# Kernel optimization log

Hardware: AMD Instinct MI355X
Metric: run time of the kernel (lower is better)

The kernel has to match this reference:

```python
import jax, jax.numpy as jnp
import numpy as np

IN_DIM = 4
H_DIM = 128
OBS_LEN = 15
PRED_LEN = 15
BATCH = 32768


def _lstm_cell(x, h, c, Wih, Whh, bih, bhh):
    # PyTorch gate order: i, f, g, o
    gates = x @ Wih.T + h @ Whh.T + (bih + bhh)  # [B, 4H]
    i, f, g, o = jnp.split(gates, 4, axis=-1)
    c_new = jax.nn.sigmoid(f) * c + jax.nn.sigmoid(i) * jnp.tanh(g)
    h_new = jax.nn.sigmoid(o) * jnp.tanh(c_new)
    return h_new, c_new


def setup_inputs() -> dict:
    key = jax.random.key(0)
    ks = jax.random.split(key, 12)
    s = 1.0 / np.sqrt(H_DIM)  # PyTorch LSTM/Linear uniform init bound
    u = lambda k, shape: jax.random.uniform(k, shape, jnp.float32, -s, s)
    return {
        "x": jax.random.normal(ks[0], (BATCH, OBS_LEN, IN_DIM), jnp.float32),
        "enc_Wih": u(ks[1], (4 * H_DIM, IN_DIM)),
        "enc_Whh": u(ks[2], (4 * H_DIM, H_DIM)),
        "enc_bih": u(ks[3], (4 * H_DIM,)),
        "enc_bhh": u(ks[4], (4 * H_DIM,)),
        "dec_Wih": u(ks[5], (4 * H_DIM, IN_DIM)),
        "dec_Whh": u(ks[6], (4 * H_DIM, H_DIM)),
        "dec_bih": u(ks[7], (4 * H_DIM,)),
        "dec_bhh": u(ks[8], (4 * H_DIM,)),
        "out_W": u(ks[9], (IN_DIM, H_DIM)),
        "out_b": u(ks[10], (IN_DIM,)),
    }


def reference(x, enc_Wih, enc_Whh, enc_bih, enc_bhh,
              dec_Wih, dec_Whh, dec_bih, dec_bhh, out_W, out_b):
    B = x.shape[0]
    h0 = jnp.zeros((B, H_DIM), x.dtype)
    c0 = jnp.zeros((B, H_DIM), x.dtype)

    # ---- encode: run LSTM over time, keep final h ----
    def enc_step(carry, xt):
        h, c = carry
        h, c = _lstm_cell(xt, h, c, enc_Wih, enc_Whh, enc_bih, enc_bhh)
        return (h, c), None

    (h_enc, _), _ = jax.lax.scan(enc_step, (h0, c0), jnp.swapaxes(x, 0, 1))

    def dec_step(carry, _):
        x0, h, c = carry
        h, c = _lstm_cell(x0, h, c, dec_Wih, dec_Whh, dec_bih, dec_bhh)
        x0 = h @ out_W.T + out_b  # [B, IN_DIM]
        return (x0, h, c), x0

    x0 = x[:, -1, :]
    _, preds = jax.lax.scan(dec_step, (x0, h_enc, h_enc), None, length=PRED_LEN)
    return jnp.swapaxes(preds, 0, 1)  # [B, PRED_LEN, IN_DIM]
```

## Files before the change

kernel.cpp:

```cpp
#include <hip/hip_runtime.h>

#define HD   128
#define SEQ  15
#define BN   32
#define LDH  168
#define KT   5
#define NTHR 512

typedef __bf16 bf16x8 __attribute__((ext_vector_type(8)));
typedef unsigned short us8 __attribute__((ext_vector_type(8)));
typedef float f32x4 __attribute__((ext_vector_type(4)));

__device__ __forceinline__ unsigned short f2bf(float f) {
  unsigned int u = __builtin_bit_cast(unsigned int, f);
  u += 0x7fffu + ((u >> 16) & 1u);
  return (unsigned short)(u >> 16);
}
__device__ __forceinline__ float bfl(unsigned int u) { return __builtin_bit_cast(float, u << 16); }
__device__ __forceinline__ float bfh(unsigned int u) { return __builtin_bit_cast(float, u & 0xffff0000u); }
__device__ __forceinline__ float sigm(float v) { return __builtin_amdgcn_rcpf(1.0f + __expf(-v)); }
__device__ __forceinline__ float tanh_(float v) { return 1.0f - 2.0f * __builtin_amdgcn_rcpf(1.0f + __expf(2.0f * v)); }

__global__ __launch_bounds__(NTHR, 2) void lstm_encdec_kernel(
    const float* __restrict__ x,
    const float* __restrict__ eWih, const float* __restrict__ eWhh,
    const float* __restrict__ ebih, const float* __restrict__ ebhh,
    const float* __restrict__ dWih, const float* __restrict__ dWhh,
    const float* __restrict__ dbih, const float* __restrict__ dbhh,
    const float* __restrict__ oW,  const float* __restrict__ ob,
    float* __restrict__ out)
{
  const int tid  = (int)threadIdx.x;
  const int wv   = tid >> 6;
  const int lane = tid & 63;
  const int l15  = lane & 15;
  const int lk   = lane >> 4;
  const int b0   = (int)blockIdx.x * BN;

  const int pv = tid >> 2, pb = pv >> 2, pd = pv & 3, pq = tid & 3;

  __shared__ alignas(16) unsigned short hb[2][BN][LDH];
  __shared__ alignas(16) unsigned short xbuf[BN][68];
  __shared__ alignas(16) float obuf[BN][68];
  __shared__ float ow_l[4][133];
  __shared__ float ob_l[4];

  bf16x8 bw[4][KT];
  f32x4  cst[2], hst[2];

  for (int i = tid; i < 2 * BN * LDH; i += NTHR) ((unsigned short*)hb)[i] = 0;
  #pragma unroll
  for (int m = 0; m < 2; ++m)
    #pragma unroll
    for (int j = 0; j < 4; ++j) { cst[m][j] = 0.0f; hst[m][j] = 0.0f; }

  auto load_w = [&](const float* Wih, const float* Whh,
                    const float* bih, const float* bhh, bool fold) {
    #pragma unroll
    for (int g = 0; g < 4; ++g) {
      const int gc = g * HD + wv * 16 + l15;
      float wi[4];
      #pragma unroll
      for (int d = 0; d < 4; ++d) wi[d] = Wih[gc * 4 + d];
      float bb = bih[gc] + bhh[gc];
      if (fold) {
        #pragma unroll
        for (int d = 0; d < 4; ++d) bb += ob[d] * wi[d];
      }
      #pragma unroll
      for (int kt = 0; kt < KT - 1; ++kt) {
        const int k0 = kt * 32 + lk * 8;
        const float4* p = (const float4*)&Whh[(size_t)gc * HD + k0];
        const float4 u0 = p[0], u1 = p[1];
        float v[8] = {u0.x, u0.y, u0.z, u0.w, u1.x, u1.y, u1.z, u1.w};
        if (fold) {
          #pragma unroll
          for (int j = 0; j < 8; ++j) {
            float s = v[j];
            #pragma unroll
            for (int d = 0; d < 4; ++d) s += wi[d] * oW[d * HD + k0 + j];
            v[j] = s;
          }
        }
        us8 u;
        #pragma unroll
        for (int j = 0; j < 8; ++j) u[j] = f2bf(v[j]);
        bw[g][kt] = __builtin_bit_cast(bf16x8, u);
      }
      us8 u4 = {0, 0, 0, 0, 0, 0, 0, 0};
      if (lk == 0) {
        #pragma unroll
        for (int j = 0; j < 4; ++j) u4[j] = f2bf(wi[j]);
        const unsigned short bh = f2bf(bb);
        u4[4] = bh;
        u4[5] = f2bf(bb - bfl((unsigned)bh));
      }
      bw[g][KT - 1] = __builtin_bit_cast(bf16x8, u4);
    }
  };

  auto mfma_step = [&](f32x4 (&acc)[2][4], int p) {
    #pragma unroll
    for (int m = 0; m < 2; ++m)
      #pragma unroll
      for (int g = 0; g < 4; ++g)
        #pragma unroll
        for (int j = 0; j < 4; ++j) acc[m][g][j] = 0.0f;
    #pragma unroll
    for (int kt = 0; kt < KT; ++kt) {
      #pragma unroll
      for (int m = 0; m < 2; ++m) {
        const bf16x8 a = __builtin_bit_cast(bf16x8,
            *(const uint4*)&hb[p][m * 16 + l15][kt * 32 + lk * 8]);
        #pragma unroll
        for (int g = 0; g < 4; ++g)
          acc[m][g] = __builtin_amdgcn_mfma_f32_16x16x32_bf16(a, bw[g][kt], acc[m][g], 0, 0, 0);
      }
    }
  };

  auto act_update = [&](f32x4 (&acc)[2][4]) {
    #pragma unroll
    for (int m = 0; m < 2; ++m)
      #pragma unroll
      for (int j = 0; j < 4; ++j) {
        const float iv = sigm(acc[m][0][j]);
        const float fv = sigm(acc[m][1][j]);
        const float gv = tanh_(acc[m][2][j]);
        const float ov = sigm(acc[m][3][j]);
        const float cv = fv * cst[m][j] + iv * gv;
        cst[m][j] = cv;
        hst[m][j] = ov * tanh_(cv);
      }
  };

  auto write_h = [&](int pw) {
    #pragma unroll
    for (int m = 0; m < 2; ++m)
      #pragma unroll
      for (int j = 0; j < 4; ++j)
        hb[pw][m * 16 + lk * 4 + j][wv * 16 + l15] = f2bf(hst[m][j]);
  };

  auto proj = [&](int p) {
    float s = 0.0f;
    #pragma unroll
    for (int c = 0; c < 4; ++c) {
      const int rc = (c + pq) & 3;
      const int k  = pq * 32 + rc * 8;
      const uint4 hv = *(const uint4*)&hb[p][pb][k];
      const float* w = &ow_l[pd][k];
      s += bfl(hv.x) * w[0] + bfh(hv.x) * w[1]
         + bfl(hv.y) * w[2] + bfh(hv.y) * w[3]
         + bfl(hv.z) * w[4] + bfh(hv.z) * w[5]
         + bfl(hv.w) * w[6] + bfh(hv.w) * w[7];
    }
    s += __shfl_xor(s, 1);
    s += __shfl_xor(s, 2);
    return s + ob_l[pd];
  };

  load_w(eWih, eWhh, ebih, ebhh, false);
  if (tid < 480) {
    const int b = tid / 15, c = tid % 15;
    const float4 xv = *(const float4*)&x[(size_t)(b0 + b) * 60 + c * 4];
    *(unsigned int*)&xbuf[b][c * 4]     = (unsigned)f2bf(xv.x) | ((unsigned)f2bf(xv.y) << 16);
    *(unsigned int*)&xbuf[b][c * 4 + 2] = (unsigned)f2bf(xv.z) | ((unsigned)f2bf(xv.w) << 16);
  }
  __syncthreads();
  if (tid < 64) {
    const int buf = tid >> 5, b = tid & 31;
    *(unsigned int*)&hb[buf][b][132] = 0x3F803F80u;
  }
  if (tid < BN) {
    const uint2 xv = *(const uint2*)&xbuf[tid][0];
    *(uint2*)&hb[0][tid][128] = xv;
  }
  __syncthreads();

  int p = 0;
  #pragma unroll 2
  for (int t = 0; t < SEQ; ++t) {
    f32x4 acc[2][4];
    mfma_step(acc, p);
    act_update(acc);
    write_h(p ^ 1);
    if (t < SEQ - 1 && tid < BN) {
      const uint2 xv = *(const uint2*)&xbuf[tid][(t + 1) * 4];
      *(uint2*)&hb[p ^ 1][tid][128] = xv;
    }
    __syncthreads();
    p ^= 1;
  }

  cst[0] = hst[0]; cst[1] = hst[1];
  load_w(dWih, dWhh, dbih, dbhh, true);
  for (int i = tid; i < 4 * HD; i += NTHR) ow_l[i >> 7][i & 127] = oW[i];
  if (tid < 4) ob_l[tid] = ob[tid];
  __syncthreads();
  {
    const float s = proj(p);
    if (pq == 0) {
      const float x14 = bfl((unsigned)xbuf[pb][56 + pd]);
      hb[p][pb][128 + pd] = f2bf(x14 - s);
    }
  }
  __syncthreads();

  #pragma unroll 2
  for (int t = 0; t < SEQ; ++t) {
    f32x4 acc[2][4];
    mfma_step(acc, p);
    if (t > 0) {
      const float pr = proj(p);
      if (pq == 0) obuf[pb][(t - 1) * 4 + pd] = pr;
    }
    act_update(acc);
    write_h(p ^ 1);
    if (tid < BN)
      *(uint2*)&hb[p ^ 1][tid][128] = (uint2){0u, 0u};
    __syncthreads();
    p ^= 1;
  }
  {
    const float pr = proj(p);
    if (pq == 0) obuf[pb][14 * 4 + pd] = pr;
  }
  __syncthreads();

  if (tid < 480) {
    const int b = tid / 15, c = tid % 15;
    const float4 v = *(const float4*)&obuf[b][c * 4];
    *(float4*)&out[(size_t)(b0 + b) * 60 + c * 4] = v;
  }
}

extern "C" void kernel_launch(void* const* d_in, const int* in_sizes, int n_in,
                              void* d_out, int out_size, void* d_ws, size_t ws_size,
                              hipStream_t stream) {
  const float* x    = (const float*)d_in[0];
  const float* eWih = (const float*)d_in[1];
  const float* eWhh = (const float*)d_in[2];
  const float* ebih = (const float*)d_in[3];
  const float* ebhh = (const float*)d_in[4];
  const float* dWih = (const float*)d_in[5];
  const float* dWhh = (const float*)d_in[6];
  const float* dbih = (const float*)d_in[7];
  const float* dbhh = (const float*)d_in[8];
  const float* oW   = (const float*)d_in[9];
  const float* ob   = (const float*)d_in[10];

  const int batch = in_sizes[0] / (SEQ * 4);
  dim3 grid(batch / BN), block(NTHR);
  lstm_encdec_kernel<<<grid, block, 0, stream>>>(
      x, eWih, eWhh, ebih, ebhh, dWih, dWhh, dbih, dbhh, oW, ob, (float*)d_out);
}
```

Measured before the change: 436.5 us.

## Halve batch tile, move input/bias term to fdot2, merge activation reciprocals

The batch tile per block shrinks from 32 to 16 rows, so each wave holds one MFMA row tile and launch bounds request 4 blocks per CU instead of 2. The input and bias contribution no longer rides in an extra K-tile of the MFMA. It is computed with packed fp16 dot2 instructions on bias-initialised accumulators, which cuts MFMA count per step from 5 to 4 K-tiles. The gate activations are rewritten to share reciprocals, and x is stored as fp16 instead of bf16. The risks are more blocks with duplicated weight loads, fp16 range and precision for inputs, and lower MFMA reuse of the weight registers.

Result: slower. 845.5 us (+93.7%).

```diff
diff --git a/kernel.cpp b/kernel.cpp
--- a/kernel.cpp
+++ b/kernel.cpp
@@ -2,14 +2,16 @@
 
 #define HD   128
 #define SEQ  15
-#define BN   32
-#define LDH  168
-#define KT   5
+#define BN   16
+#define LDH  136
+#define KT   4
 #define NTHR 512
+#define LXB  68
 
 typedef __bf16 bf16x8 __attribute__((ext_vector_type(8)));
 typedef unsigned short us8 __attribute__((ext_vector_type(8)));
 typedef float f32x4 __attribute__((ext_vector_type(4)));
+typedef _Float16 h2 __attribute__((ext_vector_type(2)));
 
 __device__ __forceinline__ unsigned short f2bf(float f) {
   unsigned int u = __builtin_bit_cast(unsigned int, f);
@@ -18,10 +20,60 @@
 }
 __device__ __forceinline__ float bfl(unsigned int u) { return __builtin_bit_cast(float, u << 16); }
 __device__ __forceinline__ float bfh(unsigned int u) { return __builtin_bit_cast(float, u & 0xffff0000u); }
-__device__ __forceinline__ float sigm(float v) { return __builtin_amdgcn_rcpf(1.0f + __expf(-v)); }
-__device__ __forceinline__ float tanh_(float v) { return 1.0f - 2.0f * __builtin_amdgcn_rcpf(1.0f + __expf(2.0f * v)); }
-
-__global__ __launch_bounds__(NTHR, 2) void lstm_encdec_kernel(
+
+__device__ __forceinline__ float dot2f(h2 a, h2 b, float c) {
+#if __has_builtin(__builtin_amdgcn_fdot2)
+  return __builtin_amdgcn_fdot2(a, b, c, false);
+#else
+  return c + (float)a[0] * (float)b[0] + (float)a[1] * (float)b[1];
+#endif
+}
+
+static __device__ __forceinline__ void load_weights(
+    const float* __restrict__ Wih, const float* __restrict__ Whh,
+    const float* __restrict__ bih, const float* __restrict__ bhh,
+    const float* __restrict__ oW,  const float* __restrict__ ob,
+    bool fold, int wv, int l15, int lk,
+    bf16x8 (&bw)[4][KT], h2 (&wih)[4][2], float (&bb)[4])
+{
+  #pragma unroll
+  for (int g = 0; g < 4; ++g) {
+    const int gc = g * HD + wv * 16 + l15;
+    float wi[4];
+    #pragma unroll
+    for (int d = 0; d < 4; ++d) wi[d] = Wih[gc * 4 + d];
+    float b = bih[gc] + bhh[gc];
+    if (fold) {
+      #pragma unroll
+      for (int d = 0; d < 4; ++d) b += ob[d] * wi[d];
+    }
+    bb[g] = b;
+    wih[g][0] = h2{(_Float16)wi[0], (_Float16)wi[1]};
+    wih[g][1] = h2{(_Float16)wi[2], (_Float16)wi[3]};
+    #pragma unroll
+    for (int kt = 0; kt < KT; ++kt) {
+      const int k0 = kt * 32 + lk * 8;
+      const float4* p = (const float4*)&Whh[(size_t)gc * HD + k0];
+      const float4 u0 = p[0], u1 = p[1];
+      float v[8] = {u0.x, u0.y, u0.z, u0.w, u1.x, u1.y, u1.z, u1.w};
+      if (fold) {
+        #pragma unroll
+        for (int j = 0; j < 8; ++j) {
+          float s = v[j];
+          #pragma unroll
+          for (int d = 0; d < 4; ++d) s += wi[d] * oW[d * HD + k0 + j];
+          v[j] = s;
+        }
+      }
+      us8 u;
+      #pragma unroll
+      for (int j = 0; j < 8; ++j) u[j] = f2bf(v[j]);
+      bw[g][kt] = __builtin_bit_cast(bf16x8, u);
+    }
+  }
+}
+
+__global__ __launch_bounds__(NTHR, 4) void lstm_encdec_kernel(
     const float* __restrict__ x,
     const float* __restrict__ eWih, const float* __restrict__ eWhh,
     const float* __restrict__ ebih, const float* __restrict__ ebhh,
@@ -32,122 +84,91 @@
 {
   const int tid  = (int)threadIdx.x;
   const int wv   = tid >> 6;
-  const int lane = tid & 63;
-  const int l15  = lane & 15;
-  const int lk   = lane >> 4;
+  const int l15  = tid & 15;
+  const int lk   = (tid & 63) >> 4;
   const int b0   = (int)blockIdx.x * BN;
-
-  const int pv = tid >> 2, pb = pv >> 2, pd = pv & 3, pq = tid & 3;
+  const int pv = tid >> 3, pb = pv >> 2, pd = pv & 3, pq = tid & 7;
 
   __shared__ alignas(16) unsigned short hb[2][BN][LDH];
-  __shared__ alignas(16) unsigned short xbuf[BN][68];
-  __shared__ alignas(16) float obuf[BN][68];
-  __shared__ float ow_l[4][133];
+  __shared__ alignas(16) unsigned short xbuf[BN][LXB];
+  __shared__ alignas(16) float obuf[BN][64];
+  __shared__ float ow_l[4][134];
   __shared__ float ob_l[4];
 
   bf16x8 bw[4][KT];
-  f32x4  cst[2], hst[2];
+  h2     wih[4][2];
+  float  bb[4];
+  f32x4  cst = {0.f, 0.f, 0.f, 0.f};
+  f32x4  hst = {0.f, 0.f, 0.f, 0.f};
 
   for (int i = tid; i < 2 * BN * LDH; i += NTHR) ((unsigned short*)hb)[i] = 0;
-  #pragma unroll
-  for (int m = 0; m < 2; ++m)
-    #pragma unroll
-    for (int j = 0; j < 4; ++j) { cst[m][j] = 0.0f; hst[m][j] = 0.0f; }
-
-  auto load_w = [&](const float* Wih, const float* Whh,
-                    const float* bih, const float* bhh, bool fold) {
-    #pragma unroll
-    for (int g = 0; g < 4; ++g) {
-      const int gc = g * HD + wv * 16 + l15;
-      float wi[4];
-      #pragma unroll
-      for (int d = 0; d < 4; ++d) wi[d] = Wih[gc * 4 + d];
-      float bb = bih[gc] + bhh[gc];
-      if (fold) {
-        #pragma unroll
-        for (int d = 0; d < 4; ++d) bb += ob[d] * wi[d];
-      }
-      #pragma unroll
-      for (int kt = 0; kt < KT - 1; ++kt) {
-        const int k0 = kt * 32 + lk * 8;
-        const float4* p = (const float4*)&Whh[(size_t)gc * HD + k0];
-        const float4 u0 = p[0], u1 = p[1];
-        float v[8] = {u0.x, u0.y, u0.z, u0.w, u1.x, u1.y, u1.z, u1.w};
-        if (fold) {
-          #pragma unroll
-          for (int j = 0; j < 8; ++j) {
-            float s = v[j];
-            #pragma unroll
-            for (int d = 0; d < 4; ++d) s += wi[d] * oW[d * HD + k0 + j];
-            v[j] = s;
-          }
-        }
-        us8 u;
-        #pragma unroll
-        for (int j = 0; j < 8; ++j) u[j] = f2bf(v[j]);
-        bw[g][kt] = __builtin_bit_cast(bf16x8, u);
-      }
-      us8 u4 = {0, 0, 0, 0, 0, 0, 0, 0};
-      if (lk == 0) {
-        #pragma unroll
-        for (int j = 0; j < 4; ++j) u4[j] = f2bf(wi[j]);
-        const unsigned short bh = f2bf(bb);
-        u4[4] = bh;
-        u4[5] = f2bf(bb - bfl((unsigned)bh));
-      }
-      bw[g][KT - 1] = __builtin_bit_cast(bf16x8, u4);
-    }
-  };
-
-  auto mfma_step = [&](f32x4 (&acc)[2][4], int p) {
-    #pragma unroll
-    for (int m = 0; m < 2; ++m)
+
+  if (tid < 240) {
+    const int b = tid / 15, c = tid % 15;
+    const float4 xv = *(const float4*)&x[(size_t)(b0 + b) * 60 + c * 4];
+    const h2 lo = {(_Float16)xv.x, (_Float16)xv.y};
+    const h2 hi = {(_Float16)xv.z, (_Float16)xv.w};
+    *(uint2*)&xbuf[b][c * 4] =
+        uint2{__builtin_bit_cast(unsigned, lo), __builtin_bit_cast(unsigned, hi)};
+  }
+
+  load_weights(eWih, eWhh, ebih, ebhh, oW, ob, false, wv, l15, lk, bw, wih, bb);
+  __syncthreads();
+
+  int p = 0;
+  for (int t = 0; t < SEQ; ++t) {
+    f32x4 acc[4];
+    #pragma unroll
+    for (int g = 0; g < 4; ++g)
+      #pragma unroll
+      for (int j = 0; j < 4; ++j) acc[g][j] = bb[g];
+    #pragma unroll
+    for (int j = 0; j < 4; ++j) {
+      const uint2 xv = *(const uint2*)&xbuf[lk * 4 + j][t * 4];
+      const h2 xlo = __builtin_bit_cast(h2, xv.x);
+      const h2 xhi = __builtin_bit_cast(h2, xv.y);
       #pragma unroll
       for (int g = 0; g < 4; ++g)
-        #pragma unroll
-        for (int j = 0; j < 4; ++j) acc[m][g][j] = 0.0f;
+        acc[g][j] = dot2f(wih[g][1], xhi, dot2f(wih[g][0], xlo, acc[g][j]));
+    }
     #pragma unroll
     for (int kt = 0; kt < KT; ++kt) {
-      #pragma unroll
-      for (int m = 0; m < 2; ++m) {
-        const bf16x8 a = __builtin_bit_cast(bf16x8,
-            *(const uint4*)&hb[p][m * 16 + l15][kt * 32 + lk * 8]);
-        #pragma unroll
-        for (int g = 0; g < 4; ++g)
-          acc[m][g] = __builtin_amdgcn_mfma_f32_16x16x32_bf16(a, bw[g][kt], acc[m][g], 0, 0, 0);
-      }
-    }
-  };
-
-  auto act_update = [&](f32x4 (&acc)[2][4]) {
-    #pragma unroll
-    for (int m = 0; m < 2; ++m)
-      #pragma unroll
-      for (int j = 0; j < 4; ++j) {
-        const float iv = sigm(acc[m][0][j]);
-        const float fv = sigm(acc[m][1][j]);
-        const float gv = tanh_(acc[m][2][j]);
-        const float ov = sigm(acc[m][3][j]);
-        const float cv = fv * cst[m][j] + iv * gv;
-        cst[m][j] = cv;
-        hst[m][j] = ov * tanh_(cv);
-      }
-  };
-
-  auto write_h = [&](int pw) {
-    #pragma unroll
-    for (int m = 0; m < 2; ++m)
-      #pragma unroll
-      for (int j = 0; j < 4; ++j)
-        hb[pw][m * 16 + lk * 4 + j][wv * 16 + l15] = f2bf(hst[m][j]);
-  };
-
-  auto proj = [&](int p) {
-    float s = 0.0f;
-    #pragma unroll
-    for (int c = 0; c < 4; ++c) {
-      const int rc = (c + pq) & 3;
-      const int k  = pq * 32 + rc * 8;
+      const bf16x8 a = __builtin_bit_cast(bf16x8,
+          *(const uint4*)&hb[p][l15][kt * 32 + lk * 8]);
+      #pragma unroll
+      for (int g = 0; g < 4; ++g)
+        acc[g] = __builtin_amdgcn_mfma_f32_16x16x32_bf16(a, bw[g][kt], acc[g], 0, 0, 0);
+    }
+    #pragma unroll
+    for (int j = 0; j < 4; ++j) {
+      const float ei = __expf(-acc[0][j]);
+      const float ef = __expf(-acc[1][j]);
+      const float eg = __expf(2.f * acc[2][j]);
+      const float eo = __expf(-acc[3][j]);
+      const float c  = cst[j] * __builtin_amdgcn_rcpf(1.f + ef)
+                     + (eg - 1.f) * __builtin_amdgcn_rcpf((1.f + ei) * (eg + 1.f));
+      cst[j] = c;
+      const float ec = __expf(2.f * c);
+      hst[j] = (ec - 1.f) * __builtin_amdgcn_rcpf((1.f + eo) * (ec + 1.f));
+    }
+    #pragma unroll
+    for (int j = 0; j < 4; ++j)
+      hb[p ^ 1][lk * 4 + j][wv * 16 + l15] = f2bf(hst[j]);
+    __syncthreads();
+    p ^= 1;
+  }
+
+  cst = hst;
+  load_weights(dWih, dWhh, dbih, dbhh, oW, ob, true, wv, l15, lk, bw, wih, bb);
+  for (int i = tid; i < 4 * HD; i += NTHR) ow_l[i >> 7][i & 127] = oW[i];
+  if (tid < 4) ob_l[tid] = ob[tid];
+  __syncthreads();
+
+  {
+    float s = 0.f;
+    #pragma unroll
+    for (int c = 0; c < 2; ++c) {
+      const int k = pq * 16 + ((c + pq) & 1) * 8;
       const uint4 hv = *(const uint4*)&hb[p][pb][k];
       const float* w = &ow_l[pd][k];
       s += bfl(hv.x) * w[0] + bfh(hv.x) * w[1]
@@ -155,80 +176,91 @@
          + bfl(hv.z) * w[4] + bfh(hv.z) * w[5]
          + bfl(hv.w) * w[6] + bfh(hv.w) * w[7];
     }
-    s += __shfl_xor(s, 1);
-    s += __shfl_xor(s, 2);
-    return s + ob_l[pd];
-  };
-
-  load_w(eWih, eWhh, ebih, ebhh, false);
-  if (tid < 480) {
-    const int b = tid / 15, c = tid % 15;
-    const float4 xv = *(const float4*)&x[(size_t)(b0 + b) * 60 + c * 4];
-    *(unsigned int*)&xbuf[b][c * 4]     = (unsigned)f2bf(xv.x) | ((unsigned)f2bf(xv.y) << 16);
-    *(unsigned int*)&xbuf[b][c * 4 + 2] = (unsigned)f2bf(xv.z) | ((unsigned)f2bf(xv.w) << 16);
-  }
-  __syncthreads();
-  if (tid < 64) {
-    const int buf = tid >> 5, b = tid & 31;
-    *(unsigned int*)&hb[buf][b][132] = 0x3F803F80u;
-  }
-  if (tid < BN) {
-    const uint2 xv = *(const uint2*)&xbuf[tid][0];
-    *(uint2*)&hb[0][tid][128] = xv;
-  }
-  __syncthreads();
-
-  int p = 0;
-  #pragma unroll 2
+    s += __shfl_xor(s, 1); s += __shfl_xor(s, 2); s += __shfl_xor(s, 4);
+    s += ob_l[pd];
+    if (pq == 0) {
+      const _Float16 x14 = __builtin_bit_cast(_Float16, xbuf[pb][56 + pd]);
+      xbuf[pb][64 + pd] = __builtin_bit_cast(unsigned short, (_Float16)((float)x14 - s));
+    }
+  }
+  __syncthreads();
+
   for (int t = 0; t < SEQ; ++t) {
-    f32x4 acc[2][4];
-    mfma_step(acc, p);
-    act_update(acc);
-    write_h(p ^ 1);
-    if (t < SEQ - 1 && tid < BN) {
-      const uint2 xv = *(const uint2*)&xbuf[tid][(t + 1) * 4];
-      *(uint2*)&hb[p ^ 1][tid][128] = xv;
-    }
+    f32x4 acc[4];
+    #pragma unroll
+    for (int g = 0; g < 4; ++g)
+      #pragma unroll
+      for (int j = 0; j < 4; ++j) acc[g][j] = bb[g];
+    if (t == 0) {
+      #pragma unroll
+      for (int j = 0; j < 4; ++j) {
+        const uint2 xv = *(const uint2*)&xbuf[lk * 4 + j][64];
+        const h2 xlo = __builtin_bit_cast(h2, xv.x);
+        const h2 xhi = __builtin_bit_cast(h2, xv.y);
+        #pragma unroll
+        for (int g = 0; g < 4; ++g)
+          acc[g][j] = dot2f(wih[g][1], xhi, dot2f(wih[g][0], xlo, acc[g][j]));
+      }
+    }
+    #pragma unroll
+    for (int kt = 0; kt < KT; ++kt) {
+      const bf16x8 a = __builtin_bit_cast(bf16x8,
+          *(const uint4*)&hb[p][l15][kt * 32 + lk * 8]);
+      #pragma unroll
+      for (int g = 0; g < 4; ++g)
+        acc[g] = __builtin_amdgcn_mfma_f32_16x16x32_bf16(a, bw[g][kt], acc[g], 0, 0, 0);
+    }
+    if (t > 0) {
+      float s = 0.f;
+      #pragma unroll
+      for (int c = 0; c < 2; ++c) {
+        const int k = pq * 16 + ((c + pq) & 1) * 8;
+        const uint4 hv = *(const uint4*)&hb[p][pb][k];
+        const float* w = &ow_l[pd][k];
+        s += bfl(hv.x) * w[0] + bfh(hv.x) * w[1]
+           + bfl(hv.y) * w[2] + bfh(hv.y) * w[3]
+           + bfl(hv.z) * w[4] + bfh(hv.z) * w[5]
+           + bfl(hv.w) * w[6] + bfh(hv.w) * w[7];
+      }
+      s += __shfl_xor(s, 1); s += __shfl_xor(s, 2); s += __shfl_xor(s, 4);
+      if (pq == 0) obuf[pb][(t - 1) * 4 + pd] = s + ob_l[pd];
+    }
+    #pragma unroll
+    for (int j = 0; j < 4; ++j) {
+      const float ei = __expf(-acc[0][j]);
+      const float ef = __expf(-acc[1][j]);
+      const float eg = __expf(2.f * acc[2][j]);
+      const float eo = __expf(-acc[3][j]);
+      const float c  = cst[j] * __builtin_amdgcn_rcpf(1.f + ef)
+                     + (eg - 1.f) * __builtin_amdgcn_rcpf((1.f + ei) * (eg + 1.f));
+      cst[j] = c;
+      const float ec = __expf(2.f * c);
+      hst[j] = (ec - 1.f) * __builtin_amdgcn_rcpf((1.f + eo) * (ec + 1.f));
+    }
+    #pragma unroll
+    for (int j = 0; j < 4; ++j)
+      hb[p ^ 1][lk * 4 + j][wv * 16 + l15] = f2bf(hst[j]);
     __syncthreads();
     p ^= 1;
   }
-
-  cst[0] = hst[0]; cst[1] = hst[1];
-  load_w(dWih, dWhh, dbih, dbhh, true);
-  for (int i = tid; i < 4 * HD; i += NTHR) ow_l[i >> 7][i & 127] = oW[i];
-  if (tid < 4) ob_l[tid] = ob[tid];
-  __syncthreads();
   {
-    const float s = proj(p);
-    if (pq == 0) {
-      const float x14 = bfl((unsigned)xbuf[pb][56 + pd]);
-      hb[p][pb][128 + pd] = f2bf(x14 - s);
-    }
-  }
-  __syncthreads();
-
-  #pragma unroll 2
-  for (int t = 0; t < SEQ; ++t) {
-    f32x4 acc[2][4];
-    mfma_step(acc, p);
-    if (t > 0) {
-      const float pr = proj(p);
-      if (pq == 0) obuf[pb][(t - 1) * 4 + pd] = pr;
-    }
-    act_update(acc);
-    write_h(p ^ 1);
-    if (tid < BN)
-      *(uint2*)&hb[p ^ 1][tid][128] = (uint2){0u, 0u};
-    __syncthreads();
-    p ^= 1;
-  }
-  {
-    const float pr = proj(p);
-    if (pq == 0) obuf[pb][14 * 4 + pd] = pr;
-  }
-  __syncthreads();
-
-  if (tid < 480) {
+    float s = 0.f;
+    #pragma unroll
+    for (int c = 0; c < 2; ++c) {
+      const int k = pq * 16 + ((c + pq) & 1) * 8;
+      const uint4 hv = *(const uint4*)&hb[p][pb][k];
+      const float* w = &ow_l[pd][k];
+      s += bfl(hv.x) * w[0] + bfh(hv.x) * w[1]
+         + bfl(hv.y) * w[2] + bfh(hv.y) * w[3]
+         + bfl(hv.z) * w[4] + bfh(hv.z) * w[5]
+         + bfl(hv.w) * w[6] + bfh(hv.w) * w[7];
+    }
+    s += __shfl_xor(s, 1); s += __shfl_xor(s, 2); s += __shfl_xor(s, 4);
+    if (pq == 0) obuf[pb][56 + pd] = s + ob_l[pd];
+  }
+  __syncthreads();
+
+  if (tid < 240) {
     const int b = tid / 15, c = tid % 15;
     const float4 v = *(const float4*)&obuf[b][c * 4];
     *(float4*)&out[(size_t)(b0 + b) * 60 + c * 4] = v;
```
